# Kernel tuning notes

Hardware: AMD Instinct MI355X
Metric: run time of the kernel (lower is better)

Reference implementation:

```python
import jax, jax.numpy as jnp
import numpy as np

BN_EPS = 1e-5


def _bn_relu(x, g, beta, mu, var):
    # x: (B, C, N); per-channel inference batchnorm + ReLU
    scale = (g / jnp.sqrt(var + BN_EPS))[None, :, None]
    shift = (beta - mu * g / jnp.sqrt(var + BN_EPS))[None, :, None]
    return jax.nn.relu(x * scale + shift)


def setup_inputs() -> dict:
    key = jax.random.key(0)
    ks = jax.random.split(key, 8)
    B, N, S, C1, C2 = 16, 4096, 1024, 256, 512
    Cin, H = C1 + C2, 256
    inp = {
        'unknown': jax.random.normal(ks[0], (B, N, 3), jnp.float32),
        'known': jax.random.normal(ks[1], (B, S, 3), jnp.float32),
        'unknow_feats': jax.random.normal(ks[2], (B, C1, N), jnp.float32),
        'known_feats': jax.random.normal(ks[3], (B, C2, S), jnp.float32),
        'W1': jax.random.normal(ks[4], (H, Cin), jnp.float32) * (1.0 / np.sqrt(Cin)),
        'b1': jnp.zeros((H,), jnp.float32),
        'g1': jnp.ones((H,), jnp.float32),
        'beta1': jnp.zeros((H,), jnp.float32),
        'mu1': jnp.zeros((H,), jnp.float32),
        'var1': jnp.ones((H,), jnp.float32),
        'W2': jax.random.normal(ks[5], (H, H), jnp.float32) * (1.0 / np.sqrt(H)),
        'b2': jnp.zeros((H,), jnp.float32),
        'g2': jnp.ones((H,), jnp.float32),
        'beta2': jnp.zeros((H,), jnp.float32),
        'mu2': jnp.zeros((H,), jnp.float32),
        'var2': jnp.ones((H,), jnp.float32),
    }
    return inp


def reference(unknown, known, unknow_feats, known_feats,
              W1, b1, g1, beta1, mu1, var1,
              W2, b2, g2, beta2, mu2, var2):
    B, N, _ = unknown.shape
    S = known.shape[1]
    kf = jnp.transpose(known_feats, (0, 2, 1))  # (B, S, C2)

    # squared pairwise distances: (B, N, S)
    d2 = (jnp.sum(unknown * unknown, -1)[:, :, None]
          + jnp.sum(known * known, -1)[:, None, :]
          - 2.0 * jnp.einsum('bnc,bsc->bns', unknown, known))
    # 3 smallest distances (ascending), matching sort + [:3]
    neg_top, idx = jax.lax.top_k(-d2, 3)          # (B, N, 3)
    dists = -neg_top
    w = 1.0 / (dists + 1e-8)
    w = w / jnp.sum(w, -1, keepdims=True)          # (B, N, 3)

    gathered = jax.vmap(lambda f, i: f[i])(kf, idx)  # (B, N, 3, C2)
    interp = jnp.sum(gathered * w[..., None], axis=2)  # (B, N, C2)

    new_feats = jnp.concatenate(
        [jnp.transpose(unknow_feats, (0, 2, 1)), interp], axis=-1)  # (B, N, C1+C2)
    x = jnp.transpose(new_feats, (0, 2, 1))  # (B, Cin, N)

    x = _bn_relu(jnp.einsum('oc,bcn->bon', W1, x) + b1[None, :, None],
                 g1, beta1, mu1, var1)
    x = _bn_relu(jnp.einsum('oc,bcn->bon', W2, x) + b2[None, :, None],
                 g2, beta2, mu2, var2)
    return x  # (B, mlp[-1], N)
```

## Files before the change

### kernel.cpp

```cpp
#include <hip/hip_runtime.h>
#include <hip/hip_bf16.h>
#include <cstdint>
#include <cstddef>

typedef _Float16 f16;
typedef _Float16 f16x8 __attribute__((ext_vector_type(8)));
typedef _Float16 f16x4 __attribute__((ext_vector_type(4)));
typedef float    f32x4 __attribute__((ext_vector_type(4)));

constexpr int Bdim = 16, Ndim = 4096, Sdim = 1024;
constexpr int C1 = 256, C2 = 512, CIN = 768, H = 256;

__device__ __forceinline__ void async16(void* l, const void* g) {
  __builtin_amdgcn_global_load_lds(
      reinterpret_cast<__attribute__((address_space(1))) char*>(
          reinterpret_cast<uintptr_t>(g)),
      reinterpret_cast<__attribute__((address_space(3))) char*>(
          reinterpret_cast<uintptr_t>(l)),
      16, 0, 0);
}

__global__ void prep_kernel(const float* __restrict__ W1, const float* __restrict__ W2,
    const float* __restrict__ b1, const float* __restrict__ g1, const float* __restrict__ be1,
    const float* __restrict__ mu1, const float* __restrict__ va1,
    const float* __restrict__ b2, const float* __restrict__ g2, const float* __restrict__ be2,
    const float* __restrict__ mu2, const float* __restrict__ va2,
    const float* __restrict__ known,
    f16* __restrict__ W1h, f16* __restrict__ W2h, f16* __restrict__ bpanel,
    float* __restrict__ s1, float* __restrict__ t1,
    float* __restrict__ s2, float* __restrict__ t2)
{
  int i = blockIdx.x * 256 + threadIdx.x;
  if (i < H * CIN) W1h[i] = (f16)W1[i];
  if (i < H * H)   W2h[i] = (f16)W2[i];
  if (i < Bdim * Sdim) {
    const float* kp = known + (size_t)i * 3;
    float kx = kp[0], ky = kp[1], kz = kp[2];
    float sk = kx * kx + ky * ky + kz * kz;
    float mx = -2.0f * kx, my = -2.0f * ky, mz = -2.0f * kz;
    f16 hx = (f16)mx, lx = (f16)(mx - (float)hx);
    f16 hy = (f16)my, ly = (f16)(my - (float)hy);
    f16 hz = (f16)mz, lz = (f16)(mz - (float)hz);
    f16 hs = (f16)sk, ls = (f16)(sk - (float)hs);
    f16* d = bpanel + (size_t)i * 24;
    d[0] = hx; d[1] = lx; d[2]  = hx; d[3]  = lx;
    d[4] = hy; d[5] = ly; d[6]  = hy; d[7]  = ly;
    d[8] = hz; d[9] = lz; d[10] = hz; d[11] = lz;
    d[12] = hs; d[13] = ls; d[14] = (f16)0.f; d[15] = (f16)0.f;
#pragma unroll
    for (int q = 16; q < 24; ++q) d[q] = (f16)0.f;
  }
  if (i < H) {
    float sc1 = g1[i] / sqrtf(va1[i] + 1e-5f);
    s1[i] = sc1; t1[i] = b1[i] * sc1 + be1[i] - mu1[i] * sc1;
    float sc2 = g2[i] / sqrtf(va2[i] + 1e-5f);
    s2[i] = sc2; t2[i] = b2[i] * sc2 + be2[i] - mu2[i] * sc2;
  }
}

__device__ __forceinline__ void top3_insert(float pd, int pi,
    float& d0, float& d1, float& d2v, int& i0, int& i1, int& i2)
{
  bool c0 = (pd < d0) || (pd == d0 && pi < i0);
  bool c1 = (pd < d1) || (pd == d1 && pi < i1);
  bool c2 = (pd < d2v) || (pd == d2v && pi < i2);
  d2v = c1 ? d1 : (c2 ? pd : d2v);
  i2  = c1 ? i1 : (c2 ? pi : i2);
  d1  = c0 ? d0 : (c1 ? pd : d1);
  i1  = c0 ? i0 : (c1 ? pi : i1);
  d0  = c0 ? pd : d0;
  i0  = c0 ? pi : i0;
}

__global__ __launch_bounds__(512)
void knn_kernel(const float* __restrict__ unknown, const f16* __restrict__ bpanel,
                int* __restrict__ idx3, float* __restrict__ w3)
{
  __shared__ f16  Blds[Sdim * 24];
  __shared__ f16  Alds[8 * 16 * 24];
  __shared__ float su_lds[8 * 16];
  __shared__ int   cnt[128];
  __shared__ float cd[128][8];
  __shared__ int   ci[128][8];

  int t = threadIdx.x;
  int b = blockIdx.y;
  int lane = t & 63, w = t >> 6;
  int r = lane & 15, g = lane >> 4;

  if (t < 128) cnt[t] = 0;

  {
    const f16* bp = bpanel + (size_t)b * Sdim * 24;
#pragma unroll
    for (int i = 0; i < 6; ++i) {
      int c = t + i * 512;
      async16((char*)Blds + c * 16, (const char*)bp + c * 16);
    }
  }

  int n0 = blockIdx.x * 128 + w * 16;
  if (lane < 16) {
    int n = n0 + lane;
    const float* up = unknown + ((size_t)b * Ndim + n) * 3;
    float x = up[0], y = up[1], z = up[2];
    su_lds[w * 16 + lane] = x * x + y * y + z * z;
    f16 hx = (f16)x, lx = (f16)(x - (float)hx);
    f16 hy = (f16)y, ly = (f16)(y - (float)hy);
    f16 hz = (f16)z, lz = (f16)(z - (float)hz);
    f16* ar = Alds + (w * 16 + lane) * 24;
    f16x8 c0 = {hx, hx, lx, lx, hy, hy, ly, ly};
    f16x8 c1 = {hz, hz, lz, lz, (f16)1.f, (f16)1.f, (f16)0.f, (f16)0.f};
    *(f16x8*)ar = c0;
    *(f16x8*)(ar + 8) = c1;
  }
  __syncthreads();

  f16x8 af = {};
  if (g < 2) af = *(const f16x8*)(Alds + (w * 16 + r) * 24 + g * 8);
  f32x4 su4;
#pragma unroll
  for (int j = 0; j < 4; ++j) su4[j] = su_lds[w * 16 + g * 4 + j];
  int boff = r * 24 + (g & 1) * 8;

  float t0_[4], t1_[4], t2_[4];
#pragma unroll
  for (int j = 0; j < 4; ++j) { t0_[j] = 1e30f; t1_[j] = 1e30f; t2_[j] = 1e30f; }

#pragma unroll 4
  for (int T = 0; T < 64; ++T) {
    f16x8 bf = *(const f16x8*)(Blds + T * 384 + boff);
    f32x4 acc = su4;
    acc = __builtin_amdgcn_mfma_f32_16x16x32_f16(af, bf, acc, 0, 0, 0);
#pragma unroll
    for (int j = 0; j < 4; ++j) {
      float d = acc[j];
      t2_[j] = __builtin_amdgcn_fmed3f(t1_[j], t2_[j], d);
      t1_[j] = __builtin_amdgcn_fmed3f(t0_[j], t1_[j], d);
      t0_[j] = fminf(t0_[j], d);
    }
  }

#pragma unroll
  for (int m = 1; m < 16; m <<= 1) {
#pragma unroll
    for (int j = 0; j < 4; ++j) {
      float b0 = __shfl_xor(t0_[j], m), b1 = __shfl_xor(t1_[j], m), b2 = __shfl_xor(t2_[j], m);
      float n0m = fminf(t0_[j], b0);
      float n1m = fminf(fmaxf(t0_[j], b0), fminf(t1_[j], b1));
      float n2m = fminf(fminf(fmaxf(t0_[j], b1), fmaxf(t1_[j], b0)), fminf(t2_[j], b2));
      t0_[j] = n0m; t1_[j] = n1m; t2_[j] = n2m;
    }
  }

#pragma unroll 2
  for (int T = 0; T < 64; ++T) {
    f16x8 bf = *(const f16x8*)(Blds + T * 384 + boff);
    f32x4 acc = su4;
    acc = __builtin_amdgcn_mfma_f32_16x16x32_f16(af, bf, acc, 0, 0, 0);
    bool h = (acc[0] <= t2_[0]) | (acc[1] <= t2_[1]) |
             (acc[2] <= t2_[2]) | (acc[3] <= t2_[3]);
    if (h) {
#pragma unroll
      for (int j = 0; j < 4; ++j) {
        if (acc[j] <= t2_[j]) {
          int q = w * 16 + g * 4 + j;
          int slot = atomicAdd(&cnt[q], 1);
          if (slot < 8) { cd[q][slot] = acc[j]; ci[q][slot] = T * 16 + r; }
        }
      }
    }
  }
  __syncthreads();

  if (t < 128) {
    int q = t;
    float d0 = 1e30f, d1 = 1e30f, d2v = 1e30f;
    int i0 = 0x7fffffff, i1 = 0x7fffffff, i2 = 0x7fffffff;
    int mc = cnt[q] < 8 ? cnt[q] : 8;
#pragma unroll
    for (int i = 0; i < 8; ++i)
      if (i < mc) top3_insert(cd[q][i], ci[q][i], d0, d1, d2v, i0, i1, i2);
    float wa = 1.0f / (d0 + 1e-8f);
    float wb = 1.0f / (d1 + 1e-8f);
    float wc = 1.0f / (d2v + 1e-8f);
    float wsum = wa + wb + wc;
    int n = blockIdx.x * 128 + q;
    int p = b * Ndim + n;
    idx3[3 * p] = i0; idx3[3 * p + 1] = i1; idx3[3 * p + 2] = i2;
    w3[3 * p] = wa / wsum; w3[3 * p + 1] = wb / wsum; w3[3 * p + 2] = wc / wsum;
  }
}

__global__ void transpose_cast(const float* __restrict__ in, f16* __restrict__ out,
                               int R, int C, int ldo, long inBStride, long outBStride)
{
  __shared__ float tile[32][33];
  const float* src = in + blockIdx.z * inBStride;
  f16* dst = out + blockIdx.z * outBStride;
  int r0 = blockIdx.y * 32, c0 = blockIdx.x * 32;
  int tx = threadIdx.x & 31, ty = threadIdx.x >> 5;
#pragma unroll
  for (int i = 0; i < 4; ++i)
    tile[ty + i * 8][tx] = src[(size_t)(r0 + ty + i * 8) * C + c0 + tx];
  __syncthreads();
#pragma unroll
  for (int i = 0; i < 4; ++i)
    dst[(size_t)(c0 + ty + i * 8) * ldo + r0 + tx] = (f16)tile[tx][ty + i * 8];
}

__global__ __launch_bounds__(256)
void interp_kernel(const f16* __restrict__ kfT, const int* __restrict__ idx3,
                   const float* __restrict__ w3, f16* __restrict__ feat)
{
  int t = threadIdx.x;
  int wv = t >> 6, l = t & 63;
  int ptbase = blockIdx.x * 32 + wv * 8;
#pragma unroll
  for (int i = 0; i < 8; ++i) {
    int pt = ptbase + i;
    int b = pt >> 12;
    int i0 = idx3[3 * pt], i1 = idx3[3 * pt + 1], i2 = idx3[3 * pt + 2];
    float w0 = w3[3 * pt], w1 = w3[3 * pt + 1], w2 = w3[3 * pt + 2];
    const f16* base = kfT + ((size_t)b << 10) * C2;
    f16x8 a = *((const f16x8*)(base + (size_t)i0 * C2) + l);
    f16x8 c = *((const f16x8*)(base + (size_t)i1 * C2) + l);
    f16x8 d = *((const f16x8*)(base + (size_t)i2 * C2) + l);
    f16x8 o;
#pragma unroll
    for (int j = 0; j < 8; ++j)
      o[j] = (f16)(w0 * (float)a[j] + w1 * (float)c[j] + w2 * (float)d[j]);
    *((f16x8*)(feat + (size_t)pt * CIN + C1) + l) = o;
  }
}

template <int K, int MODE>
__global__ __launch_bounds__(256)
void gemm_kernel(const f16* __restrict__ A, const f16* __restrict__ Bt,
                 const float* __restrict__ scale, const float* __restrict__ shift,
                 void* __restrict__ outp)
{
  __shared__ char lds[65536];

  int id = blockIdx.x;
  id = (id & 7) * 128 + (id >> 3);
  int big = id >> 1, small = id & 1;
  int m0, n0;
  if (MODE == 1) { m0 = small * 128; n0 = big * 128; }
  else           { m0 = big * 128;  n0 = small * 128; }

  int t = threadIdx.x;
  int lane = t & 63, wid = t >> 6;
  int wm = wid >> 1, wn = wid & 1;
  int lr = lane & 15, lh = lane >> 4;

  f32x4 acc[4][4] = {};

  constexpr int NT = K / 64;
  const f16* Arow = A + (size_t)m0 * K;
  const f16* Brow = Bt + (size_t)n0 * K;
  int p = t >> 3, x = t & 7;

  auto STAGE = [&](int buf, int kt) {
    int k0 = kt * 64;
    char* base = lds + buf * 32768;
#pragma unroll
    for (int r = 0; r < 4; ++r) {
      int row = r * 32 + p;
      int sw = (x ^ (row & 7)) * 8;
      async16(base + r * 4096 + t * 16,         Arow + (size_t)row * K + k0 + sw);
      async16(base + 16384 + r * 4096 + t * 16, Brow + (size_t)row * K + k0 + sw);
    }
  };

  STAGE(0, 0);
  __syncthreads();
  int cur = 0;
  for (int kt = 0; kt < NT; ++kt) {
    if (kt + 1 < NT) STAGE(cur ^ 1, kt + 1);
    const char* Ab = lds + cur * 32768;
    const char* Bb = Ab + 16384;
#pragma unroll
    for (int kk = 0; kk < 2; ++kk) {
      f16x8 af[4], bf[4];
#pragma unroll
      for (int mf = 0; mf < 4; ++mf) {
        int row = wm * 64 + mf * 16 + lr;
        int g = kk * 4 + lh;
        af[mf] = *(const f16x8*)(Ab + row * 128 + ((g ^ (row & 7)) << 4));
      }
#pragma unroll
      for (int nf = 0; nf < 4; ++nf) {
        int row = wn * 64 + nf * 16 + lr;
        int g = kk * 4 + lh;
        bf[nf] = *(const f16x8*)(Bb + row * 128 + ((g ^ (row & 7)) << 4));
      }
#pragma unroll
      for (int mf = 0; mf < 4; ++mf)
#pragma unroll
        for (int nf = 0; nf < 4; ++nf)
          acc[mf][nf] = __builtin_amdgcn_mfma_f32_16x16x32_f16(af[mf], bf[nf], acc[mf][nf], 0, 0, 0);
    }
    __syncthreads();
    cur ^= 1;
  }

  if (MODE == 1) {
    f16* x1 = (f16*)outp;
#pragma unroll
    for (int mf = 0; mf < 4; ++mf) {
      int ob = m0 + wm * 64 + mf * 16 + lh * 4;
      f32x4 sc = *(const f32x4*)(scale + ob);
      f32x4 sh = *(const f32x4*)(shift + ob);
#pragma unroll
      for (int nf = 0; nf < 4; ++nf) {
        int ptc = n0 + wn * 64 + nf * 16 + lr;
        f16x4 v;
#pragma unroll
        for (int j = 0; j < 4; ++j) {
          float y = acc[mf][nf][j] * sc[j] + sh[j];
          v[j] = (f16)(y > 0.0f ? y : 0.0f);
        }
        *(f16x4*)(x1 + (size_t)ptc * H + ob) = v;
      }
    }
  } else {
    float* out = (float*)outp;
#pragma unroll
    for (int mf = 0; mf < 4; ++mf) {
      int ptb = m0 + wm * 64 + mf * 16 + lh * 4;
      int bb = ptb >> 12, nn = ptb & 4095;
#pragma unroll
      for (int nf = 0; nf < 4; ++nf) {
        int o = n0 + wn * 64 + nf * 16 + lr;
        float sc = scale[o], sh = shift[o];
        f32x4 v;
#pragma unroll
        for (int j = 0; j < 4; ++j) {
          float y = acc[mf][nf][j] * sc + sh;
          v[j] = (y > 0.0f ? y : 0.0f);
        }
        *(f32x4*)(out + ((size_t)(bb * H + o) << 12) + nn) = v;
      }
    }
  }
}

extern "C" void kernel_launch(void* const* d_in, const int* in_sizes, int n_in,
                              void* d_out, int out_size, void* d_ws, size_t ws_size,
                              hipStream_t stream)
{
  (void)in_sizes; (void)n_in; (void)out_size; (void)ws_size;
  const float* unknown = (const float*)d_in[0];
  const float* known   = (const float*)d_in[1];
  const float* uf      = (const float*)d_in[2];
  const float* kf      = (const float*)d_in[3];
  const float* W1  = (const float*)d_in[4];
  const float* b1  = (const float*)d_in[5];
  const float* g1  = (const float*)d_in[6];
  const float* be1 = (const float*)d_in[7];
  const float* mu1 = (const float*)d_in[8];
  const float* va1 = (const float*)d_in[9];
  const float* W2  = (const float*)d_in[10];
  const float* b2  = (const float*)d_in[11];
  const float* g2  = (const float*)d_in[12];
  const float* be2 = (const float*)d_in[13];
  const float* mu2 = (const float*)d_in[14];
  const float* va2 = (const float*)d_in[15];

  char* ws = (char*)d_ws;
  f16*   W1h    = (f16*)(ws + 0);
  f16*   W2h    = (f16*)(ws + 393216);
  float* s1     = (float*)(ws + 524288);
  float* t1     = (float*)(ws + 525312);
  float* s2     = (float*)(ws + 526336);
  float* t2     = (float*)(ws + 527360);
  int*   idx3   = (int*)(ws + 528384);
  float* w3     = (float*)(ws + 1314816);
  f16*   bpanel = (f16*)(ws + 2101248);
  f16*   kfT    = (f16*)(ws + 2887680);
  f16*   feat   = (f16*)(ws + 19664896);
  f16*   x1     = (f16*)(ws + 120328192);

  prep_kernel<<<768, 256, 0, stream>>>(W1, W2, b1, g1, be1, mu1, va1,
                                       b2, g2, be2, mu2, va2, known,
                                       W1h, W2h, bpanel, s1, t1, s2, t2);
  knn_kernel<<<dim3(Ndim / 128, Bdim), 512, 0, stream>>>(unknown, bpanel, idx3, w3);
  transpose_cast<<<dim3(Sdim / 32, C2 / 32, Bdim), 256, 0, stream>>>(
      kf, kfT, C2, Sdim, C2, (long)C2 * Sdim, (long)Sdim * C2);
  transpose_cast<<<dim3(Ndim / 32, C1 / 32, Bdim), 256, 0, stream>>>(
      uf, feat, C1, Ndim, CIN, (long)C1 * Ndim, (long)Ndim * CIN);
  interp_kernel<<<(Bdim * Ndim) / 32, 256, 0, stream>>>(kfT, idx3, w3, feat);
  gemm_kernel<CIN, 1><<<1024, 256, 0, stream>>>(W1h, feat, s1, t1, x1);
  gemm_kernel<H,   2><<<1024, 256, 0, stream>>>(x1, W2h, s2, t2, d_out);
}
```

Measured before the change: 308.3 us.

## Fuse three-neighbor interpolation into first GEMM's B-tile staging

Removes the separate interp kernel and the materialised 768-channel feature buffer. The first GEMM now stages the unknown-feature part of B through async LDS loads and builds the interpolated part directly in LDS from gathered kfT rows and weights during the K loop. This cuts the write and reread of the large feature tensor. The cost is synchronous gathers and conversion work inside the GEMM pipeline, and the interpolation is recomputed by both M-tile blocks that share an N tile.

```diff
diff --git a/kernel.cpp b/kernel.cpp
--- a/kernel.cpp
+++ b/kernel.cpp
@@ -210,44 +210,147 @@
 }
 
 __global__ __launch_bounds__(256)
-void interp_kernel(const f16* __restrict__ kfT, const int* __restrict__ idx3,
-                   const float* __restrict__ w3, f16* __restrict__ feat)
-{
-  int t = threadIdx.x;
-  int wv = t >> 6, l = t & 63;
-  int ptbase = blockIdx.x * 32 + wv * 8;
-#pragma unroll
-  for (int i = 0; i < 8; ++i) {
-    int pt = ptbase + i;
-    int b = pt >> 12;
-    int i0 = idx3[3 * pt], i1 = idx3[3 * pt + 1], i2 = idx3[3 * pt + 2];
-    float w0 = w3[3 * pt], w1 = w3[3 * pt + 1], w2 = w3[3 * pt + 2];
-    const f16* base = kfT + ((size_t)b << 10) * C2;
-    f16x8 a = *((const f16x8*)(base + (size_t)i0 * C2) + l);
-    f16x8 c = *((const f16x8*)(base + (size_t)i1 * C2) + l);
-    f16x8 d = *((const f16x8*)(base + (size_t)i2 * C2) + l);
-    f16x8 o;
-#pragma unroll
-    for (int j = 0; j < 8; ++j)
-      o[j] = (f16)(w0 * (float)a[j] + w1 * (float)c[j] + w2 * (float)d[j]);
-    *((f16x8*)(feat + (size_t)pt * CIN + C1) + l) = o;
-  }
-}
-
-template <int K, int MODE>
-__global__ __launch_bounds__(256)
-void gemm_kernel(const f16* __restrict__ A, const f16* __restrict__ Bt,
+void gemm1_fused(const f16* __restrict__ W1h, const f16* __restrict__ ufT,
+                 const f16* __restrict__ kfT, const int* __restrict__ idx3,
+                 const float* __restrict__ w3,
                  const float* __restrict__ scale, const float* __restrict__ shift,
-                 void* __restrict__ outp)
+                 f16* __restrict__ x1)
 {
   __shared__ char lds[65536];
 
   int id = blockIdx.x;
   id = (id & 7) * 128 + (id >> 3);
   int big = id >> 1, small = id & 1;
-  int m0, n0;
-  if (MODE == 1) { m0 = small * 128; n0 = big * 128; }
-  else           { m0 = big * 128;  n0 = small * 128; }
+  int m0 = small * 128;
+  int n0 = big * 128;
+  int b  = n0 >> 12;
+
+  int t = threadIdx.x;
+  int lane = t & 63, wid = t >> 6;
+  int wm = wid >> 1, wn = wid & 1;
+  int lr = lane & 15, lh = lane >> 4;
+  int p = t >> 3, x = t & 7;
+
+  int ptl = t >> 1, qq = t & 1;
+  int pg = n0 + ptl;
+  int ia = idx3[3 * pg], ib = idx3[3 * pg + 1], ic = idx3[3 * pg + 2];
+  float w0 = w3[3 * pg], w1 = w3[3 * pg + 1], w2 = w3[3 * pg + 2];
+  const f16* kb = kfT + ((size_t)b << 10) * C2;
+  const f16* r0p = kb + (size_t)ia * C2 + qq * 32;
+  const f16* r1p = kb + (size_t)ib * C2 + qq * 32;
+  const f16* r2p = kb + (size_t)ic * C2 + qq * 32;
+
+  const f16* Arow = W1h + (size_t)m0 * CIN;
+  const f16* Brow = ufT + (size_t)n0 * C1;
+
+  auto STAGE_A = [&](int buf, int kt) {
+    int k0 = kt * 64;
+    char* base = lds + buf * 32768;
+#pragma unroll
+    for (int r = 0; r < 4; ++r) {
+      int row = r * 32 + p;
+      int sw = (x ^ (row & 7)) * 8;
+      async16(base + r * 4096 + t * 16, Arow + (size_t)row * CIN + k0 + sw);
+    }
+  };
+  auto STAGE_B_uf = [&](int buf, int kt) {
+    int k0 = kt * 64;
+    char* base = lds + buf * 32768 + 16384;
+#pragma unroll
+    for (int r = 0; r < 4; ++r) {
+      int row = r * 32 + p;
+      int sw = (x ^ (row & 7)) * 8;
+      async16(base + r * 4096 + t * 16, Brow + (size_t)row * C1 + k0 + sw);
+    }
+  };
+  auto STAGE_B_interp = [&](int buf, int kt) {
+    char* base = lds + buf * 32768 + 16384;
+    int e0 = (kt - 4) * 64;
+#pragma unroll
+    for (int i = 0; i < 4; ++i) {
+      int g = qq * 4 + i;
+      f16x8 a = *(const f16x8*)(r0p + e0 + i * 8);
+      f16x8 c = *(const f16x8*)(r1p + e0 + i * 8);
+      f16x8 d = *(const f16x8*)(r2p + e0 + i * 8);
+      f16x8 o;
+#pragma unroll
+      for (int j = 0; j < 8; ++j)
+        o[j] = (f16)(w0 * (float)a[j] + w1 * (float)c[j] + w2 * (float)d[j]);
+      *(f16x8*)(base + ptl * 128 + ((g ^ (ptl & 7)) << 4)) = o;
+    }
+  };
+
+  f32x4 acc[4][4] = {};
+
+  STAGE_A(0, 0);
+  STAGE_B_uf(0, 0);
+  __syncthreads();
+#pragma unroll
+  for (int kt = 0; kt < 12; ++kt) {
+    int cb = kt & 1, nb = cb ^ 1;
+    if (kt + 1 < 12) {
+      STAGE_A(nb, kt + 1);
+      if (kt + 1 < 4) STAGE_B_uf(nb, kt + 1);
+      else            STAGE_B_interp(nb, kt + 1);
+    }
+    const char* Ab = lds + cb * 32768;
+    const char* Bb = Ab + 16384;
+#pragma unroll
+    for (int kk = 0; kk < 2; ++kk) {
+      f16x8 af[4], bf[4];
+#pragma unroll
+      for (int mf = 0; mf < 4; ++mf) {
+        int row = wm * 64 + mf * 16 + lr;
+        int g = kk * 4 + lh;
+        af[mf] = *(const f16x8*)(Ab + row * 128 + ((g ^ (row & 7)) << 4));
+      }
+#pragma unroll
+      for (int nf = 0; nf < 4; ++nf) {
+        int row = wn * 64 + nf * 16 + lr;
+        int g = kk * 4 + lh;
+        bf[nf] = *(const f16x8*)(Bb + row * 128 + ((g ^ (row & 7)) << 4));
+      }
+#pragma unroll
+      for (int mf = 0; mf < 4; ++mf)
+#pragma unroll
+        for (int nf = 0; nf < 4; ++nf)
+          acc[mf][nf] = __builtin_amdgcn_mfma_f32_16x16x32_f16(af[mf], bf[nf], acc[mf][nf], 0, 0, 0);
+    }
+    __syncthreads();
+  }
+
+#pragma unroll
+  for (int mf = 0; mf < 4; ++mf) {
+    int ob = m0 + wm * 64 + mf * 16 + lh * 4;
+    f32x4 sc = *(const f32x4*)(scale + ob);
+    f32x4 sh = *(const f32x4*)(shift + ob);
+#pragma unroll
+    for (int nf = 0; nf < 4; ++nf) {
+      int ptc = n0 + wn * 64 + nf * 16 + lr;
+      f16x4 v;
+#pragma unroll
+      for (int j = 0; j < 4; ++j) {
+        float y = acc[mf][nf][j] * sc[j] + sh[j];
+        v[j] = (f16)(y > 0.0f ? y : 0.0f);
+      }
+      *(f16x4*)(x1 + (size_t)ptc * H + ob) = v;
+    }
+  }
+}
+
+template <int K>
+__global__ __launch_bounds__(256)
+void gemm2_kernel(const f16* __restrict__ A, const f16* __restrict__ Bt,
+                  const float* __restrict__ scale, const float* __restrict__ shift,
+                  float* __restrict__ out)
+{
+  __shared__ char lds[65536];
+
+  int id = blockIdx.x;
+  id = (id & 7) * 128 + (id >> 3);
+  int big = id >> 1, small = id & 1;
+  int m0 = big * 128;
+  int n0 = small * 128;
 
   int t = threadIdx.x;
   int lane = t & 63, wid = t >> 6;
@@ -305,43 +408,21 @@
     cur ^= 1;
   }
 
-  if (MODE == 1) {
-    f16* x1 = (f16*)outp;
-#pragma unroll
-    for (int mf = 0; mf < 4; ++mf) {
-      int ob = m0 + wm * 64 + mf * 16 + lh * 4;
-      f32x4 sc = *(const f32x4*)(scale + ob);
-      f32x4 sh = *(const f32x4*)(shift + ob);
-#pragma unroll
-      for (int nf = 0; nf < 4; ++nf) {
-        int ptc = n0 + wn * 64 + nf * 16 + lr;
-        f16x4 v;
-#pragma unroll
-        for (int j = 0; j < 4; ++j) {
-          float y = acc[mf][nf][j] * sc[j] + sh[j];
-          v[j] = (f16)(y > 0.0f ? y : 0.0f);
-        }
-        *(f16x4*)(x1 + (size_t)ptc * H + ob) = v;
-      }
-    }
-  } else {
-    float* out = (float*)outp;
-#pragma unroll
-    for (int mf = 0; mf < 4; ++mf) {
-      int ptb = m0 + wm * 64 + mf * 16 + lh * 4;
-      int bb = ptb >> 12, nn = ptb & 4095;
-#pragma unroll
-      for (int nf = 0; nf < 4; ++nf) {
-        int o = n0 + wn * 64 + nf * 16 + lr;
-        float sc = scale[o], sh = shift[o];
-        f32x4 v;
-#pragma unroll
-        for (int j = 0; j < 4; ++j) {
-          float y = acc[mf][nf][j] * sc + sh;
-          v[j] = (y > 0.0f ? y : 0.0f);
-        }
-        *(f32x4*)(out + ((size_t)(bb * H + o) << 12) + nn) = v;
-      }
+#pragma unroll
+  for (int mf = 0; mf < 4; ++mf) {
+    int ptb = m0 + wm * 64 + mf * 16 + lh * 4;
+    int bb = ptb >> 12, nn = ptb & 4095;
+#pragma unroll
+    for (int nf = 0; nf < 4; ++nf) {
+      int o = n0 + wn * 64 + nf * 16 + lr;
+      float sc = scale[o], sh = shift[o];
+      f32x4 v;
+#pragma unroll
+      for (int j = 0; j < 4; ++j) {
+        float y = acc[mf][nf][j] * sc + sh;
+        v[j] = (y > 0.0f ? y : 0.0f);
+      }
+      *(f32x4*)(out + ((size_t)(bb * H + o) << 12) + nn) = v;
     }
   }
 }
@@ -379,8 +460,8 @@
   float* w3     = (float*)(ws + 1314816);
   f16*   bpanel = (f16*)(ws + 2101248);
   f16*   kfT    = (f16*)(ws + 2887680);
-  f16*   feat   = (f16*)(ws + 19664896);
-  f16*   x1     = (f16*)(ws + 120328192);
+  f16*   ufT    = (f16*)(ws + 19664896);
+  f16*   x1     = (f16*)(ws + 53219328);
 
   prep_kernel<<<768, 256, 0, stream>>>(W1, W2, b1, g1, be1, mu1, va1,
                                        b2, g2, be2, mu2, va2, known,
@@ -389,8 +470,7 @@
   transpose_cast<<<dim3(Sdim / 32, C2 / 32, Bdim), 256, 0, stream>>>(
       kf, kfT, C2, Sdim, C2, (long)C2 * Sdim, (long)Sdim * C2);
   transpose_cast<<<dim3(Ndim / 32, C1 / 32, Bdim), 256, 0, stream>>>(
-      uf, feat, C1, Ndim, CIN, (long)C1 * Ndim, (long)Ndim * CIN);
-  interp_kernel<<<(Bdim * Ndim) / 32, 256, 0, stream>>>(kfT, idx3, w3, feat);
-  gemm_kernel<CIN, 1><<<1024, 256, 0, stream>>>(W1h, feat, s1, t1, x1);
-  gemm_kernel<H,   2><<<1024, 256, 0, stream>>>(x1, W2h, s2, t2, d_out);
-}
+      uf, ufT, C1, Ndim, C1, (long)C1 * Ndim, (long)Ndim * C1);
+  gemm1_fused<<<1024, 256, 0, stream>>>(W1h, ufT, kfT, idx3, w3, s1, t1, x1);
+  gemm2_kernel<H><<<1024, 256, 0, stream>>>(x1, W2h, s2, t2, (float*)d_out);
+}
```

Result: faster. 301.0 us (-2.3%).
